# Performance work log

Hardware: AMD Instinct MI355X
Metric: run time of the kernel (lower is better)

## Reference

```python
import jax, jax.numpy as jnp
import numpy as np

NUM_HEAD = 16
DIM = 1024
T, B = 2048, 4


def setup_inputs() -> dict:
    key = jax.random.key(0)
    ks = jax.random.split(key, 12)
    s = 1.0 / np.sqrt(DIM)
    return {
        "x1": jax.random.normal(ks[0], (T, B, DIM), jnp.float32),
        "x2": jax.random.normal(ks[1], (T, B, DIM), jnp.float32),
        "Wq": jax.random.normal(ks[2], (DIM, DIM), jnp.float32) * s,
        "bq": jax.random.normal(ks[3], (DIM,), jnp.float32) * 0.01,
        "Wk": jax.random.normal(ks[4], (DIM, DIM), jnp.float32) * s,
        "bk": jax.random.normal(ks[5], (DIM,), jnp.float32) * 0.01,
        "Wv": jax.random.normal(ks[6], (DIM, DIM), jnp.float32) * s,
        "bv": jax.random.normal(ks[7], (DIM,), jnp.float32) * 0.01,
        "Wu": jax.random.normal(ks[8], (DIM, DIM), jnp.float32) * s,
        "bu": jax.random.normal(ks[9], (DIM,), jnp.float32) * 0.01,
    }


def reference(x1, x2, Wq, bq, Wk, bk, Wv, bv, Wu, bu):
    T1, B1, C = x1.shape
    T2 = x2.shape[0]
    H = NUM_HEAD
    hd = C // H
    # (T,B,C) -> (B,T,C)
    x1b = jnp.transpose(x1, (1, 0, 2))
    x2b = jnp.transpose(x2, (1, 0, 2))
    # torch Linear: y = x @ W.T + b
    q = (x1b @ Wq.T + bq).reshape(B1, T1, H, hd).transpose(0, 2, 1, 3)  # (B,H,T1,hd)
    k = (x2b @ Wk.T + bk).reshape(B1, T2, H, hd).transpose(0, 2, 1, 3)
    v = (x2b @ Wv.T + bv).reshape(B1, T2, H, hd).transpose(0, 2, 1, 3)
    # NOTE: source scales by 1/sqrt(C) (full dim), not 1/sqrt(head_dim)
    attn = jnp.einsum("bhqd,bhkd->bhqk", q, k) / jnp.sqrt(jnp.asarray(C, q.dtype))
    attn = jax.nn.softmax(attn, axis=-1)
    # dropout = identity (eval mode, deterministic reference)
    out = jnp.einsum("bhqk,bhkd->bhqd", attn, v)  # (B,H,T1,hd)
    out = out.transpose(0, 2, 1, 3).reshape(B1, T1, C)  # merge heads
    out = out @ Wu.T + bu
    return out
```

## Files before the change

kernel.cpp:

```cpp
#include <hip/hip_runtime.h>

#define TSEQ 2048
#define BB 4
#define CDIM 1024
#define NH 16
#define HD 64
#define MR (TSEQ*BB)
#define C2SCALE 0.045084220f

typedef __attribute__((ext_vector_type(8))) short sh8;
typedef __attribute__((ext_vector_type(4))) short sh4;
typedef __attribute__((ext_vector_type(4))) float f4;

__device__ __forceinline__ unsigned short f2bf(float x){
  unsigned u = __builtin_bit_cast(unsigned, x);
  u += 0x7fffu + ((u>>16)&1u);
  return (unsigned short)(u>>16);
}

__device__ __forceinline__ unsigned pk2(float a, float b){
  unsigned ua = __builtin_bit_cast(unsigned, a) + 0x8000u;
  unsigned ub = __builtin_bit_cast(unsigned, b) + 0x8000u;
  return __builtin_amdgcn_perm(ua, ub, 0x07060302u);
}

__device__ __forceinline__ void gll16(const unsigned short* g, unsigned short* l){
  __builtin_amdgcn_global_load_lds(
      (const __attribute__((address_space(1))) unsigned int*)g,
      (__attribute__((address_space(3))) unsigned int*)l, 16, 0, 0);
}

__global__ void conv_x(const float* __restrict__ a, const float* __restrict__ b,
                       unsigned short* __restrict__ ya, unsigned short* __restrict__ yb){
  const float* s = blockIdx.y ? b : a;
  unsigned short* d = blockIdx.y ? yb : ya;
  int i = (blockIdx.x*256 + threadIdx.x)*4;
  f4 v = *(const f4*)(s+i);
  sh4 o;
  o.x = (short)f2bf(v.x); o.y = (short)f2bf(v.y);
  o.z = (short)f2bf(v.z); o.w = (short)f2bf(v.w);
  *(sh4*)(d+i) = o;
}

__global__ void conv_w(const float* __restrict__ w0, const float* __restrict__ w1,
                       const float* __restrict__ w2, const float* __restrict__ w3,
                       unsigned short* __restrict__ y0, unsigned short* __restrict__ y1,
                       unsigned short* __restrict__ y2, unsigned short* __restrict__ y3){
  const float* s; unsigned short* d;
  switch(blockIdx.y){
    case 0: s=w0; d=y0; break;
    case 1: s=w1; d=y1; break;
    case 2: s=w2; d=y2; break;
    default: s=w3; d=y3; break;
  }
  int i = (blockIdx.x*256 + threadIdx.x)*4;
  f4 v = *(const f4*)(s+i);
  sh4 o;
  o.x = (short)f2bf(v.x); o.y = (short)f2bf(v.y);
  o.z = (short)f2bf(v.z); o.w = (short)f2bf(v.w);
  *(sh4*)(d+i) = o;
}

__global__ __launch_bounds__(256,2) void gemm_u(
    const unsigned short* __restrict__ A, const unsigned short* __restrict__ Bw,
    const float* __restrict__ bias, float* __restrict__ Cout){
  __shared__ unsigned short As[128*32];
  __shared__ unsigned short Bs[128*32];
  const int tid  = threadIdx.x;
  const int wave = tid>>6, lane = tid&63;
  const int g = lane>>4, c = lane&15;
  const int m0 = blockIdx.x*128, n0 = blockIdx.y*128;
  const int wr = wave>>1, wc = wave&1;
  f4 acc[4][4] = {};
  const int r0 = tid>>2, cc0 = tid&3;
  const unsigned short* Ag = A  + (size_t)(m0+r0)*CDIM + cc0*8;
  const unsigned short* Bg = Bw + (size_t)(n0+r0)*CDIM + cc0*8;

  for (int k0=0; k0<CDIM; k0+=32){
    __syncthreads();
    gll16(Ag + k0,                    As + tid*8);
    gll16(Ag + (size_t)64*CDIM + k0,  As + (256+tid)*8);
    gll16(Bg + k0,                    Bs + tid*8);
    gll16(Bg + (size_t)64*CDIM + k0,  Bs + (256+tid)*8);
    __syncthreads();
    sh8 af[4], bfr[4];
#pragma unroll
    for (int mt=0; mt<4; mt++) af[mt]  = *(const sh8*)(As + (wr*64+mt*16+c)*32 + g*8);
#pragma unroll
    for (int nt=0; nt<4; nt++) bfr[nt] = *(const sh8*)(Bs + (wc*64+nt*16+c)*32 + g*8);
#pragma unroll
    for (int mt=0; mt<4; mt++)
#pragma unroll
      for (int nt=0; nt<4; nt++)
        acc[mt][nt] = __builtin_amdgcn_mfma_f32_16x16x32_bf16(af[mt], bfr[nt], acc[mt][nt], 0,0,0);
  }

#pragma unroll
  for (int nt=0; nt<4; nt++){
    int nn = n0 + wc*64 + nt*16 + c;
    float bsv = bias[nn];
#pragma unroll
    for (int mt=0; mt<4; mt++){
      int mb = m0 + wr*64 + mt*16 + 4*g;
#pragma unroll
      for (int r=0; r<4; r++)
        Cout[(size_t)(mb+r)*CDIM + nn] = acc[mt][nt][r] + bsv;
    }
  }
}

__global__ __launch_bounds__(256,2) void gemm_qkv(
    const unsigned short* __restrict__ x1b, const unsigned short* __restrict__ x2b,
    const unsigned short* __restrict__ wq, const unsigned short* __restrict__ wk,
    const unsigned short* __restrict__ wv,
    const float* __restrict__ bq, const float* __restrict__ bk, const float* __restrict__ bv,
    unsigned short* __restrict__ Qo, unsigned short* __restrict__ Ko,
    unsigned short* __restrict__ Vo){
  __shared__ unsigned short As[128*32];
  __shared__ unsigned short Bs[128*32];
  const int z = blockIdx.z;
  const unsigned short* A  = (z==0) ? x1b : x2b;
  const unsigned short* Bw = (z==0) ? wq : (z==1) ? wk : wv;
  const float* bias        = (z==0) ? bq : (z==1) ? bk : bv;
  const int tid  = threadIdx.x;
  const int wave = tid>>6, lane = tid&63;
  const int g = lane>>4, c = lane&15;
  const int m0 = blockIdx.x*128, n0 = blockIdx.y*128;
  const int wr = wave>>1, wc = wave&1;
  f4 acc[4][4] = {};
  const int r0 = tid>>2, cc0 = tid&3;
  const unsigned short* Ag = A  + (size_t)(m0+r0)*CDIM + cc0*8;
  const unsigned short* Bg = Bw + (size_t)(n0+r0)*CDIM + cc0*8;

  for (int k0=0; k0<CDIM; k0+=32){
    __syncthreads();
    gll16(Ag + k0,                    As + tid*8);
    gll16(Ag + (size_t)64*CDIM + k0,  As + (256+tid)*8);
    gll16(Bg + k0,                    Bs + tid*8);
    gll16(Bg + (size_t)64*CDIM + k0,  Bs + (256+tid)*8);
    __syncthreads();
    sh8 af[4], bfr[4];
#pragma unroll
    for (int mt=0; mt<4; mt++) af[mt]  = *(const sh8*)(As + (wr*64+mt*16+c)*32 + g*8);
#pragma unroll
    for (int nt=0; nt<4; nt++) bfr[nt] = *(const sh8*)(Bs + (wc*64+nt*16+c)*32 + g*8);
#pragma unroll
    for (int mt=0; mt<4; mt++)
#pragma unroll
      for (int nt=0; nt<4; nt++)
        acc[mt][nt] = __builtin_amdgcn_mfma_f32_16x16x32_bf16(af[mt], bfr[nt], acc[mt][nt], 0,0,0);
  }

#pragma unroll
  for (int nt=0; nt<4; nt++){
    int nn = n0 + wc*64 + nt*16 + c;
    float bsv = bias[nn];
#pragma unroll
    for (int mt=0; mt<4; mt++){
      int mb = m0 + wr*64 + mt*16 + 4*g;
#pragma unroll
      for (int r=0; r<4; r++){
        float v = acc[mt][nt][r] + bsv;
        int mm = mb + r;
        if (z==0){
          Qo[(size_t)mm*CDIM + nn] = f2bf(v*C2SCALE);
        } else if (z==1){
          Ko[(size_t)mm*CDIM + nn] = f2bf(v);
        } else {
          int t = mm>>2, bb = mm&3, h = nn>>6, d = nn&63;
          Vo[(((size_t)bb*NH + h)*HD + d)*TSEQ + t] = f2bf(v);
        }
      }
    }
  }
}

__global__ __launch_bounds__(256,3) void attn_kernel(
    const unsigned short* __restrict__ Q, const unsigned short* __restrict__ Kb,
    const unsigned short* __restrict__ Vt, unsigned short* __restrict__ O){
  __shared__ unsigned short Ks[128*64];
  __shared__ unsigned short Vs[64*128];
  __shared__ unsigned short Ps[4][32*64];
  const int tid=threadIdx.x, wave=tid>>6, lane=tid&63;
  const int g=lane>>4, c=lane&15;
  const int gx = blockIdx.x;
  const int bh = ((gx>>7)<<3) | (gx&7);
  const int qt = (gx>>3)&15;
  const int b = bh>>4, h = bh&15;
  const int qbase = qt*128 + wave*32;

  const unsigned short* kbase[4];
  const unsigned short* vbase[4];
#pragma unroll
  for (int i=0; i<4; i++){
    int cc = i*256+tid;
    int krow = cc>>3, kch = (cc&7) ^ (krow&7);
    kbase[i] = Kb + ((size_t)krow*BB + b)*CDIM + h*HD + kch*8;
    int vd = cc>>4, vch = (cc&15) ^ (vd&15);
    vbase[i] = Vt + ((size_t)(b*NH+h)*HD + vd)*TSEQ + vch*8;
  }

  sh8 qfr[2][2];
#pragma unroll
  for (int qf=0; qf<2; qf++)
#pragma unroll
    for (int kc=0; kc<2; kc++){
      int t = qbase + qf*16 + c;
      qfr[qf][kc] = *(const sh8*)(Q + ((size_t)t*BB + b)*CDIM + h*HD + kc*32 + g*8);
    }

  f4 oacc[4][2] = {};
  float lrun[2] = {0.f, 0.f};

  f4 kreg[4], vreg[4];
#pragma unroll
  for (int i=0; i<4; i++){
    kreg[i] = *(const f4*)(kbase[i]);
    vreg[i] = *(const f4*)(vbase[i]);
  }
#pragma unroll
  for (int i=0; i<4; i++){
    *(f4*)(Ks + (i*256+tid)*8) = kreg[i];
    *(f4*)(Vs + (i*256+tid)*8) = vreg[i];
  }
  __syncthreads();

  for (int iter=0; iter<TSEQ/128; iter++){
    if (iter < TSEQ/128-1){
      int k0n = (iter+1)*128;
#pragma unroll
      for (int i=0; i<4; i++){
        kreg[i] = *(const f4*)(kbase[i] + (size_t)k0n*BB*CDIM);
        vreg[i] = *(const f4*)(vbase[i] + k0n);
      }
    }

    f4 sacc[8][2] = {};
#pragma unroll
    for (int kf=0; kf<8; kf++){
      sh8 af[2];
#pragma unroll
      for (int kc=0; kc<2; kc++){
        int ch = (kc*4+g) ^ (c&7);
        af[kc] = *(const sh8*)(Ks + (kf*16+c)*64 + ch*8);
      }
#pragma unroll
      for (int kc=0; kc<2; kc++)
#pragma unroll
        for (int qf=0; qf<2; qf++)
          sacc[kf][qf] = __builtin_amdgcn_mfma_f32_16x16x32_bf16(af[kc], qfr[qf][kc], sacc[kf][qf],0,0,0);
    }

#pragma unroll
    for (int half=0; half<2; half++){
#pragma unroll
      for (int qf=0; qf<2; qf++){
        unsigned short* prow = Ps[wave] + (qf*16+c)*64;
#pragma unroll
        for (int kfl=0; kfl<4; kfl++){
          int kf = half*4 + kfl;
          float p0 = __builtin_amdgcn_exp2f(sacc[kf][qf][0]);
          float p1 = __builtin_amdgcn_exp2f(sacc[kf][qf][1]);
          float p2 = __builtin_amdgcn_exp2f(sacc[kf][qf][2]);
          float p3 = __builtin_amdgcn_exp2f(sacc[kf][qf][3]);
          lrun[qf] += (p0+p1)+(p2+p3);
          uint2 pr; pr.x = pk2(p1, p0); pr.y = pk2(p3, p2);
          int js = (kfl*4+g) ^ (c&14);
          *(uint2*)(prow + js*4) = pr;
        }
      }
#pragma unroll
      for (int kc2l=0; kc2l<2; kc2l++){
        int kc2 = half*2 + kc2l;
        sh8 pf[2];
#pragma unroll
        for (int qf=0; qf<2; qf++){
          int j0 = kc2l*8 + 2*g;
          pf[qf] = *(const sh8*)(Ps[wave] + (qf*16+c)*64 + ((j0 ^ (c&14)))*4);
        }
#pragma unroll
        for (int df=0; df<4; df++){
          int ch = (kc2*4+g) ^ c;
          sh8 vf = *(const sh8*)(Vs + (df*16+c)*128 + ch*8);
#pragma unroll
          for (int qf=0; qf<2; qf++)
            oacc[df][qf] = __builtin_amdgcn_mfma_f32_16x16x32_bf16(vf, pf[qf], oacc[df][qf],0,0,0);
        }
      }
    }

    __syncthreads();
    if (iter < TSEQ/128-1){
#pragma unroll
      for (int i=0; i<4; i++){
        *(f4*)(Ks + (i*256+tid)*8) = kreg[i];
        *(f4*)(Vs + (i*256+tid)*8) = vreg[i];
      }
      __syncthreads();
    }
  }

#pragma unroll
  for (int qf=0; qf<2; qf++){
    lrun[qf] += __shfl_xor(lrun[qf], 16, 64);
    lrun[qf] += __shfl_xor(lrun[qf], 32, 64);
    float inv = 1.0f/lrun[qf];
    int t = qbase + qf*16 + c;
#pragma unroll
    for (int df=0; df<4; df++){
      uint2 pr;
      pr.x = pk2(oacc[df][qf][1]*inv, oacc[df][qf][0]*inv);
      pr.y = pk2(oacc[df][qf][3]*inv, oacc[df][qf][2]*inv);
      *(uint2*)(O + ((size_t)b*TSEQ + t)*CDIM + h*HD + df*16 + 4*g) = pr;
    }
  }
}

extern "C" void kernel_launch(void* const* d_in, const int* in_sizes, int n_in,
                              void* d_out, int out_size, void* d_ws, size_t ws_size,
                              hipStream_t stream){
  (void)in_sizes; (void)n_in; (void)out_size; (void)ws_size;
  const float* x1 = (const float*)d_in[0];
  const float* x2 = (const float*)d_in[1];
  const float* Wq = (const float*)d_in[2];
  const float* bq = (const float*)d_in[3];
  const float* Wk = (const float*)d_in[4];
  const float* bk = (const float*)d_in[5];
  const float* Wv = (const float*)d_in[6];
  const float* bv = (const float*)d_in[7];
  const float* Wu = (const float*)d_in[8];
  const float* bu = (const float*)d_in[9];

  unsigned short* ws = (unsigned short*)d_ws;
  size_t o = 0;
  unsigned short* x1b = ws + o; o += (size_t)MR*CDIM;
  unsigned short* x2b = ws + o; o += (size_t)MR*CDIM;
  unsigned short* wqb = ws + o; o += (size_t)CDIM*CDIM;
  unsigned short* wkb = ws + o; o += (size_t)CDIM*CDIM;
  unsigned short* wvb = ws + o; o += (size_t)CDIM*CDIM;
  unsigned short* wub = ws + o; o += (size_t)CDIM*CDIM;
  unsigned short* Qb  = ws + o; o += (size_t)MR*CDIM;
  unsigned short* Kbf = ws + o; o += (size_t)MR*CDIM;
  unsigned short* Vtb = ws + o; o += (size_t)MR*CDIM;
  unsigned short* Ob  = x1b;

  conv_x<<<dim3((MR*CDIM)/1024, 2),   256, 0, stream>>>(x1, x2, x1b, x2b);
  conv_w<<<dim3((CDIM*CDIM)/1024, 4), 256, 0, stream>>>(Wq, Wk, Wv, Wu, wqb, wkb, wvb, wub);

  gemm_qkv<<<dim3(MR/128, CDIM/128, 3), 256, 0, stream>>>(
      x1b, x2b, wqb, wkb, wvb, bq, bk, bv, Qb, Kbf, Vtb);
  attn_kernel<<<dim3(1024), 256, 0, stream>>>(Qb, Kbf, Vtb, Ob);
  gemm_u<<<dim3(MR/128, CDIM/128), 256, 0, stream>>>(Ob, wub, bu, (float*)d_out);
}
```

Measured before the change: 352.7 us.

## Keep softmax probabilities in registers via lane permutes instead of LDS round-trip

Removes the per-wave LDS staging buffer for P. The S-tile MFMA is now split into halves interleaved with the PV step, and the bf16-packed probabilities are rearranged into the MFMA B-operand layout with v_permlane32_swap and ds_swizzle. The goal is to cut LDS writes and reads, cut LDS usage (which may allow higher occupancy), and shrink the sacc register footprint. It also adds s_setprio around the MFMA blocks to favour matrix issue across waves. The cost is that correctness depends on the lane permutation matching the old LDS layout exactly.

```diff
diff --git a/kernel.cpp b/kernel.cpp
--- a/kernel.cpp
+++ b/kernel.cpp
@@ -11,6 +11,7 @@
 typedef __attribute__((ext_vector_type(8))) short sh8;
 typedef __attribute__((ext_vector_type(4))) short sh4;
 typedef __attribute__((ext_vector_type(4))) float f4;
+typedef __attribute__((ext_vector_type(4))) unsigned int u32x4;
 
 __device__ __forceinline__ unsigned short f2bf(float x){
   unsigned u = __builtin_bit_cast(unsigned, x);
@@ -180,9 +181,9 @@
     const unsigned short* __restrict__ Vt, unsigned short* __restrict__ O){
   __shared__ unsigned short Ks[128*64];
   __shared__ unsigned short Vs[64*128];
-  __shared__ unsigned short Ps[4][32*64];
   const int tid=threadIdx.x, wave=tid>>6, lane=tid&63;
   const int g=lane>>4, c=lane&15;
+  const bool godd = (g&1);
   const int gx = blockIdx.x;
   const int bh = ((gx>>7)<<3) | (gx&7);
   const int qt = (gx>>3)&15;
@@ -235,49 +236,62 @@
       }
     }
 
-    f4 sacc[8][2] = {};
-#pragma unroll
-    for (int kf=0; kf<8; kf++){
-      sh8 af[2];
-#pragma unroll
-      for (int kc=0; kc<2; kc++){
-        int ch = (kc*4+g) ^ (c&7);
-        af[kc] = *(const sh8*)(Ks + (kf*16+c)*64 + ch*8);
-      }
-#pragma unroll
-      for (int kc=0; kc<2; kc++)
-#pragma unroll
-        for (int qf=0; qf<2; qf++)
-          sacc[kf][qf] = __builtin_amdgcn_mfma_f32_16x16x32_bf16(af[kc], qfr[qf][kc], sacc[kf][qf],0,0,0);
-    }
-
 #pragma unroll
     for (int half=0; half<2; half++){
-#pragma unroll
-      for (int qf=0; qf<2; qf++){
-        unsigned short* prow = Ps[wave] + (qf*16+c)*64;
-#pragma unroll
-        for (int kfl=0; kfl<4; kfl++){
-          int kf = half*4 + kfl;
-          float p0 = __builtin_amdgcn_exp2f(sacc[kf][qf][0]);
-          float p1 = __builtin_amdgcn_exp2f(sacc[kf][qf][1]);
-          float p2 = __builtin_amdgcn_exp2f(sacc[kf][qf][2]);
-          float p3 = __builtin_amdgcn_exp2f(sacc[kf][qf][3]);
-          lrun[qf] += (p0+p1)+(p2+p3);
-          uint2 pr; pr.x = pk2(p1, p0); pr.y = pk2(p3, p2);
-          int js = (kfl*4+g) ^ (c&14);
-          *(uint2*)(prow + js*4) = pr;
+      f4 sacc[4][2] = {};
+      __builtin_amdgcn_s_setprio(1);
+#pragma unroll
+      for (int kfl=0; kfl<4; kfl++){
+        int kf = half*4 + kfl;
+        sh8 af[2];
+#pragma unroll
+        for (int kc=0; kc<2; kc++){
+          int ch = (kc*4+g) ^ (c&7);
+          af[kc] = *(const sh8*)(Ks + (kf*16+c)*64 + ch*8);
         }
-      }
+#pragma unroll
+        for (int kc=0; kc<2; kc++)
+#pragma unroll
+          for (int qf=0; qf<2; qf++)
+            sacc[kfl][qf] = __builtin_amdgcn_mfma_f32_16x16x32_bf16(af[kc], qfr[qf][kc], sacc[kfl][qf],0,0,0);
+      }
+      __builtin_amdgcn_s_setprio(0);
+
 #pragma unroll
       for (int kc2l=0; kc2l<2; kc2l++){
-        int kc2 = half*2 + kc2l;
+        const int kc2 = half*2 + kc2l;
         sh8 pf[2];
 #pragma unroll
         for (int qf=0; qf<2; qf++){
-          int j0 = kc2l*8 + 2*g;
-          pf[qf] = *(const sh8*)(Ps[wave] + (qf*16+c)*64 + ((j0 ^ (c&14)))*4);
+          f4 sa = sacc[2*kc2l][qf];
+          f4 sb = sacc[2*kc2l+1][qf];
+          float pa0 = __builtin_amdgcn_exp2f(sa[0]);
+          float pa1 = __builtin_amdgcn_exp2f(sa[1]);
+          float pa2 = __builtin_amdgcn_exp2f(sa[2]);
+          float pa3 = __builtin_amdgcn_exp2f(sa[3]);
+          float pb0 = __builtin_amdgcn_exp2f(sb[0]);
+          float pb1 = __builtin_amdgcn_exp2f(sb[1]);
+          float pb2 = __builtin_amdgcn_exp2f(sb[2]);
+          float pb3 = __builtin_amdgcn_exp2f(sb[3]);
+          lrun[qf] += ((pa0+pa1)+(pa2+pa3)) + ((pb0+pb1)+(pb2+pb3));
+          unsigned A0 = pk2(pa1, pa0);
+          unsigned A1 = pk2(pa3, pa2);
+          unsigned B0 = pk2(pb1, pb0);
+          unsigned B1 = pk2(pb3, pb2);
+          asm("v_permlane32_swap_b32 %0, %1" : "+v"(A0), "+v"(B0));
+          asm("v_permlane32_swap_b32 %0, %1" : "+v"(A1), "+v"(B1));
+          unsigned xA0 = (unsigned)__builtin_amdgcn_ds_swizzle((int)A0, 0x401F);
+          unsigned xA1 = (unsigned)__builtin_amdgcn_ds_swizzle((int)A1, 0x401F);
+          unsigned xB0 = (unsigned)__builtin_amdgcn_ds_swizzle((int)B0, 0x401F);
+          unsigned xB1 = (unsigned)__builtin_amdgcn_ds_swizzle((int)B1, 0x401F);
+          u32x4 pw;
+          pw.x = godd ? xB0 : A0;
+          pw.y = godd ? xB1 : A1;
+          pw.z = godd ? B0  : xA0;
+          pw.w = godd ? B1  : xA1;
+          pf[qf] = __builtin_bit_cast(sh8, pw);
         }
+        __builtin_amdgcn_s_setprio(1);
 #pragma unroll
         for (int df=0; df<4; df++){
           int ch = (kc2*4+g) ^ c;
@@ -286,6 +300,7 @@
           for (int qf=0; qf<2; qf++)
             oacc[df][qf] = __builtin_amdgcn_mfma_f32_16x16x32_bf16(vf, pf[qf], oacc[df][qf],0,0,0);
         }
+        __builtin_amdgcn_s_setprio(0);
       }
     }
 
```

Result: faster. 330.8 us (-6.2%).
